# Performance work log

Measured on AMD Instinct MI355X. Metric: run time of the kernel, lower is better.

The kernel has to match this reference:

```python
import jax, jax.numpy as jnp
import numpy as np

N_SRC0, N_DST0 = 400000, 100000
N_DST1 = 25000


def _graph_conv(x_src, src, dst, n_dst, W, b):
    # DGL GraphConv, norm='both': h_v = d_in(v)^-1/2 * sum_{u->v} d_out(u)^-1/2 * x_u @ W + b
    ones = jnp.ones(src.shape[0], dtype=x_src.dtype)
    out_deg = jax.ops.segment_sum(ones, src, num_segments=x_src.shape[0])
    in_deg = jax.ops.segment_sum(ones, dst, num_segments=n_dst)
    cs = jnp.where(out_deg > 0, out_deg ** -0.5, 0.0).astype(x_src.dtype)
    cd = jnp.where(in_deg > 0, in_deg ** -0.5, 0.0).astype(x_src.dtype)
    msg = (x_src * cs[:, None])[src]                      # [E, d_in] gather
    agg = jax.ops.segment_sum(msg, dst, num_segments=n_dst)  # [n_dst, d_in] scatter-add
    return (agg * cd[:, None]) @ W + b


def setup_inputs() -> dict:
    key = jax.random.key(0)
    ks = jax.random.split(key, 8)
    E0, E1 = 3200000, 800000
    return {
        "x": jax.random.normal(ks[0], (N_SRC0, 128), dtype=jnp.float32),
        "src0": jax.random.randint(ks[1], (E0,), 0, N_SRC0, dtype=jnp.int32),
        "dst0": jax.random.randint(ks[2], (E0,), 0, N_DST0, dtype=jnp.int32),
        "src1": jax.random.randint(ks[3], (E1,), 0, N_DST0, dtype=jnp.int32),
        "dst1": jax.random.randint(ks[4], (E1,), 0, N_DST1, dtype=jnp.int32),
        "W0": jax.random.normal(ks[5], (128, 256), dtype=jnp.float32) * (128 ** -0.5),
        "b0": jnp.zeros((256,), dtype=jnp.float32),
        "W1": jax.random.normal(ks[6], (256, 64), dtype=jnp.float32) * (256 ** -0.5),
        "b1": jnp.zeros((64,), dtype=jnp.float32),
    }


def reference(x, src0, dst0, src1, dst1, W0, b0, W1, b1):
    h = jax.nn.relu(_graph_conv(x, src0, dst0, N_DST0, W0, b0))   # [N_DST0, 256]
    h = jax.nn.relu(_graph_conv(h, src1, dst1, N_DST1, W1, b1))   # [N_DST1, 64]
    return h
```

## Files before the change

### kernel.cpp

```cpp
#include <hip/hip_runtime.h>
#include <hip/hip_bf16.h>
#include <stdint.h>

#define N_SRC0 400000
#define N_DST0 100000
#define N_DST1 25000

#define SH_D0 9
#define NK_D0 196
#define SH_S0 9
#define NK_S0 782
#define SH_D1 8
#define NK_D1 98
#define SH_S1 9
#define NK_S1 196
#define NB0 1024
#define NB1 256

#define BH_D0 0
#define BH_S0 (NK_D0 * NB0)
#define BH_D1 (BH_S0 + NK_S0 * NB0)
#define BH_S1 (BH_D1 + NK_D1 * NB1)
#define BH_TOT (BH_S1 + NK_S1 * NB1)

typedef __attribute__((ext_vector_type(8))) short short8;
typedef __attribute__((ext_vector_type(4))) float f32x4;

__device__ __forceinline__ unsigned short f2bf(float f) {
    __hip_bfloat16 h = __float2bfloat16(f);
    union { __hip_bfloat16 h; unsigned short u; } c;
    c.h = h;
    return c.u;
}
__device__ __forceinline__ float bfu_lo(uint32_t u) { return __uint_as_float(u << 16); }
__device__ __forceinline__ float bfu_hi(uint32_t u) { return __uint_as_float(u & 0xffff0000u); }
__device__ __forceinline__ uint32_t packbf2(float a, float b) {
    return (uint32_t)f2bf(a) | ((uint32_t)f2bf(b) << 16);
}

__global__ __launch_bounds__(256) void part_hist2(
        const int* __restrict__ src, const int* __restrict__ dst, int n,
        int sshift, int snb, int dshift, int dnb, int NB,
        int* __restrict__ bhd, int* __restrict__ bhs) {
    extern __shared__ int h[];
    const int blk = blockIdx.x;
    for (int i = threadIdx.x; i < dnb + snb; i += 256) h[i] = 0;
    __syncthreads();
    const int per = (n + NB - 1) / NB;
    const int b = blk * per;
    const int e = min(b + per, n);
    for (int i = b + threadIdx.x; i < e; i += 256) {
        atomicAdd(&h[dst[i] >> dshift], 1);
        atomicAdd(&h[dnb + (src[i] >> sshift)], 1);
    }
    __syncthreads();
    for (int i = threadIdx.x; i < dnb; i += 256) bhd[(size_t)i * NB + blk] = h[i];
    for (int i = threadIdx.x; i < snb; i += 256) bhs[(size_t)i * NB + blk] = h[dnb + i];
}

#define SCAN_ITEMS 8
#define SCAN_TILE 2048

__global__ __launch_bounds__(256) void scan1_kernel(
        const int* __restrict__ in, int* __restrict__ out,
        int* __restrict__ sums, int n) {
    __shared__ int lds[256];
    const int tid = threadIdx.x;
    const int base = blockIdx.x * SCAN_TILE + tid * SCAN_ITEMS;
    int v[SCAN_ITEMS];
    int run = 0;
    #pragma unroll
    for (int i = 0; i < SCAN_ITEMS; ++i) {
        int t = (base + i < n) ? in[base + i] : 0;
        v[i] = run;
        run += t;
    }
    lds[tid] = run;
    __syncthreads();
    int incl = run;
    for (int off = 1; off < 256; off <<= 1) {
        int u = (tid >= off) ? lds[tid - off] : 0;
        __syncthreads();
        incl += u;
        lds[tid] = incl;
        __syncthreads();
    }
    if (tid == 255) sums[blockIdx.x] = incl;
    int excl = incl - run;
    #pragma unroll
    for (int i = 0; i < SCAN_ITEMS; ++i)
        if (base + i < n) out[base + i] = excl + v[i];
}

__global__ __launch_bounds__(256) void scan2_kernel(int* __restrict__ sums, int nb) {
    __shared__ int lds[256];
    const int tid = threadIdx.x;
    const int base = tid * 4;
    int v[4];
    int run = 0;
    #pragma unroll
    for (int i = 0; i < 4; ++i) {
        int t = (base + i < nb) ? sums[base + i] : 0;
        v[i] = run;
        run += t;
    }
    lds[tid] = run;
    __syncthreads();
    int incl = run;
    for (int off = 1; off < 256; off <<= 1) {
        int u = (tid >= off) ? lds[tid - off] : 0;
        __syncthreads();
        incl += u;
        lds[tid] = incl;
        __syncthreads();
    }
    int excl = incl - run;
    #pragma unroll
    for (int i = 0; i < 4; ++i)
        if (base + i < nb) sums[base + i] = excl + v[i];
}

__global__ void scan3_kernel(int* __restrict__ out, const int* __restrict__ sums, int n) {
    int i = blockIdx.x * blockDim.x + threadIdx.x;
    if (i < n) out[i] += sums[i / SCAN_TILE];
}

__global__ __launch_bounds__(256) void part_scat2(
        const int* __restrict__ src, const int* __restrict__ dst, int n,
        int sshift, int snb, int dshift, int dnb, int NB,
        const int* __restrict__ bhd, const int* __restrict__ bhs,
        uint64_t* __restrict__ stg) {
    extern __shared__ int cur[];
    const int blk = blockIdx.x;
    for (int i = threadIdx.x; i < dnb; i += 256) cur[i] = bhd[(size_t)i * NB + blk];
    for (int i = threadIdx.x; i < snb; i += 256) cur[dnb + i] = bhs[(size_t)i * NB + blk];
    __syncthreads();
    const int per = (n + NB - 1) / NB;
    const int b = blk * per;
    const int e = min(b + per, n);
    for (int i = b + threadIdx.x; i < e; i += 256) {
        int s = src[i], d = dst[i];
        int pd = atomicAdd(&cur[d >> dshift], 1);
        stg[pd] = ((uint64_t)(uint32_t)d << 32) | (uint32_t)s;
        int ps = atomicAdd(&cur[dnb + (s >> sshift)], 1);
        stg[ps] = ((uint64_t)(uint32_t)s << 32);
    }
}

__global__ __launch_bounds__(256) void fine_csr(
        const uint64_t* __restrict__ stg, const int* __restrict__ bhs,
        int NB, int shift, int nbins, int total, int rel,
        int* __restrict__ off, int* __restrict__ esrc) {
    __shared__ int fine[512];
    __shared__ int part[256];
    const int k = blockIdx.x;
    const int fb = 1 << shift;
    const int base = bhs[(size_t)k * NB];
    const int end = (k + 1 < gridDim.x) ? bhs[(size_t)(k + 1) * NB] : total;
    const int gb = k << shift;
    const int t = threadIdx.x;
    for (int i = t; i < fb; i += 256) fine[i] = 0;
    __syncthreads();
    for (int i = base + t; i < end; i += 256)
        atomicAdd(&fine[(int)(stg[i] >> 32) - gb], 1);
    __syncthreads();
    int a0 = (2 * t < fb) ? fine[2 * t] : 0;
    int a1 = (2 * t + 1 < fb) ? fine[2 * t + 1] : 0;
    part[t] = a0 + a1;
    __syncthreads();
    int incl = part[t];
    for (int o = 1; o < 256; o <<= 1) {
        int u = (t >= o) ? part[t - o] : 0;
        __syncthreads();
        incl += u;
        part[t] = incl;
        __syncthreads();
    }
    int excl = incl - (a0 + a1);
    if (2 * t < fb) fine[2 * t] = excl;
    if (2 * t + 1 < fb) fine[2 * t + 1] = excl + a0;
    __syncthreads();
    const int rb = base - rel;
    for (int i = t; i < fb; i += 256) {
        int g = gb + i;
        if (g < nbins) off[g] = rb + fine[i];
    }
    if (k == gridDim.x - 1 && t == 0) off[nbins] = total - rel;
    __syncthreads();
    for (int i = base + t; i < end; i += 256) {
        uint64_t pr = stg[i];
        int d = (int)(pr >> 32);
        int p = atomicAdd(&fine[d - gb], 1);
        esrc[rb + p] = (int)(uint32_t)pr;
    }
}

__global__ __launch_bounds__(256) void fine_hist(
        const uint64_t* __restrict__ stg, const int* __restrict__ bhs,
        int NB, int shift, int nbins, int total, float* __restrict__ cs) {
    __shared__ int fine[512];
    const int k = blockIdx.x;
    const int fb = 1 << shift;
    const int base = bhs[(size_t)k * NB];
    const int end = (k + 1 < gridDim.x) ? bhs[(size_t)(k + 1) * NB] : total;
    const int gb = k << shift;
    for (int i = threadIdx.x; i < fb; i += 256) fine[i] = 0;
    __syncthreads();
    for (int i = base + threadIdx.x; i < end; i += 256)
        atomicAdd(&fine[(int)(stg[i] >> 32) - gb], 1);
    __syncthreads();
    for (int i = threadIdx.x; i < fb; i += 256) {
        int g = gb + i;
        if (g < nbins) {
            int c = fine[i];
            cs[g] = c > 0 ? rsqrtf((float)c) : 0.f;
        }
    }
}

__global__ __launch_bounds__(256) void prescale_kernel(
        const float4* __restrict__ x4, const float* __restrict__ cs,
        uint2* __restrict__ xs) {
    int id = blockIdx.x * 256 + threadIdx.x;
    int row = id >> 5;
    float c = cs[row];
    float4 v = x4[id];
    uint2 o;
    o.x = packbf2(v.x * c, v.y * c);
    o.y = packbf2(v.z * c, v.w * c);
    xs[id] = o;
}

__global__ void packW0_kernel(const float* __restrict__ W, unsigned short* __restrict__ Bp) {
    int id = blockIdx.x * 256 + threadIdx.x;
    int kk = id & 31, n = (id >> 5) & 255, kt = id >> 13;
    Bp[id] = f2bf(W[(kt * 32 + kk) * 256 + n]);
}
__global__ void packW1_kernel(const float* __restrict__ W, unsigned short* __restrict__ Bp) {
    int id = blockIdx.x * 256 + threadIdx.x;
    int kk = id & 31, n = (id >> 5) & 63, kt = id >> 11;
    Bp[id] = f2bf(W[(kt * 32 + kk) * 64 + n]);
}

__global__ __launch_bounds__(256) void agg0_kernel(
        const uint32_t* __restrict__ xs, const int* __restrict__ esrc,
        const int* __restrict__ off, uint32_t* __restrict__ aggb, int nrows) {
    int row = blockIdx.x * 4 + (threadIdx.x >> 6);
    int t = threadIdx.x & 63;
    if (row >= nrows) return;
    int b = off[row], e = off[row + 1];
    float a0 = 0.f, a1 = 0.f;
    int i = b;
    for (; i + 7 < e; i += 8) {
        int s0 = esrc[i],     s1 = esrc[i + 1], s2 = esrc[i + 2], s3 = esrc[i + 3];
        int s4 = esrc[i + 4], s5 = esrc[i + 5], s6 = esrc[i + 6], s7 = esrc[i + 7];
        uint32_t u0 = xs[(size_t)s0 * 64 + t];
        uint32_t u1 = xs[(size_t)s1 * 64 + t];
        uint32_t u2 = xs[(size_t)s2 * 64 + t];
        uint32_t u3 = xs[(size_t)s3 * 64 + t];
        uint32_t u4 = xs[(size_t)s4 * 64 + t];
        uint32_t u5 = xs[(size_t)s5 * 64 + t];
        uint32_t u6 = xs[(size_t)s6 * 64 + t];
        uint32_t u7 = xs[(size_t)s7 * 64 + t];
        a0 += ((bfu_lo(u0) + bfu_lo(u1)) + (bfu_lo(u2) + bfu_lo(u3)))
            + ((bfu_lo(u4) + bfu_lo(u5)) + (bfu_lo(u6) + bfu_lo(u7)));
        a1 += ((bfu_hi(u0) + bfu_hi(u1)) + (bfu_hi(u2) + bfu_hi(u3)))
            + ((bfu_hi(u4) + bfu_hi(u5)) + (bfu_hi(u6) + bfu_hi(u7)));
    }
    for (; i < e; ++i) {
        uint32_t u = xs[(size_t)esrc[i] * 64 + t];
        a0 += bfu_lo(u);
        a1 += bfu_hi(u);
    }
    float cd = (e > b) ? rsqrtf((float)(e - b)) : 0.f;
    aggb[(size_t)row * 64 + t] = packbf2(a0 * cd, a1 * cd);
}

__global__ __launch_bounds__(256) void gemm0_mfma(
        const short* __restrict__ A,
        const short* __restrict__ Bp,
        const float* __restrict__ bias,
        unsigned short* __restrict__ H) {
    const int w = threadIdx.x >> 6;
    const int l = threadIdx.x & 63;
    const int rbase = blockIdx.x * 32;
    const int cbase = w * 64;
    const int lr = l & 15;
    const int lk = (l >> 4) * 8;
    f32x4 acc[2][4] = {};
    #pragma unroll
    for (int kt = 0; kt < 4; ++kt) {
        short8 a[2], b[4];
        #pragma unroll
        for (int rt = 0; rt < 2; ++rt)
            a[rt] = *(const short8*)(A + (size_t)(rbase + rt * 16 + lr) * 128 + kt * 32 + lk);
        #pragma unroll
        for (int ct = 0; ct < 4; ++ct)
            b[ct] = *(const short8*)(Bp + (size_t)(kt * 256 + cbase + ct * 16 + lr) * 32 + lk);
        #pragma unroll
        for (int rt = 0; rt < 2; ++rt)
            #pragma unroll
            for (int ct = 0; ct < 4; ++ct)
                acc[rt][ct] = __builtin_amdgcn_mfma_f32_16x16x32_bf16(a[rt], b[ct], acc[rt][ct], 0, 0, 0);
    }
    const int orow0 = (l >> 4) * 4;
    #pragma unroll
    for (int rt = 0; rt < 2; ++rt) {
        #pragma unroll
        for (int ct = 0; ct < 4; ++ct) {
            int col = cbase + ct * 16 + lr;
            float bv = bias[col];
            #pragma unroll
            for (int j = 0; j < 4; ++j) {
                int row = rbase + rt * 16 + orow0 + j;
                float v = fmaxf(acc[rt][ct][j] + bv, 0.f);
                H[(size_t)row * 256 + col] = f2bf(v);
            }
        }
    }
}

__global__ __launch_bounds__(256) void gemmt_mfma(
        const short* __restrict__ A,
        const short* __restrict__ Bp,
        const float* __restrict__ cs1,
        unsigned short* __restrict__ Y,
        int M) {
    const int w = threadIdx.x >> 6;
    const int l = threadIdx.x & 63;
    const int rbase = blockIdx.x * 128 + w * 32;
    const int lr = l & 15;
    const int lk = (l >> 4) * 8;
    f32x4 acc[2][4] = {};
    #pragma unroll
    for (int kt = 0; kt < 8; ++kt) {
        short8 a[2], b[4];
        #pragma unroll
        for (int rt = 0; rt < 2; ++rt)
            a[rt] = *(const short8*)(A + (size_t)(rbase + rt * 16 + lr) * 256 + kt * 32 + lk);
        #pragma unroll
        for (int ct = 0; ct < 4; ++ct)
            b[ct] = *(const short8*)(Bp + (size_t)(kt * 64 + ct * 16 + lr) * 32 + lk);
        #pragma unroll
        for (int rt = 0; rt < 2; ++rt)
            #pragma unroll
            for (int ct = 0; ct < 4; ++ct)
                acc[rt][ct] = __builtin_amdgcn_mfma_f32_16x16x32_bf16(a[rt], b[ct], acc[rt][ct], 0, 0, 0);
    }
    const int orow0 = (l >> 4) * 4;
    #pragma unroll
    for (int rt = 0; rt < 2; ++rt) {
        #pragma unroll
        for (int j = 0; j < 4; ++j) {
            int row = rbase + rt * 16 + orow0 + j;
            if (row < M) {
                float c = cs1[row];
                #pragma unroll
                for (int ct = 0; ct < 4; ++ct) {
                    int col = ct * 16 + lr;
                    Y[(size_t)row * 64 + col] = f2bf(acc[rt][ct][j] * c);
                }
            }
        }
    }
}

__global__ __launch_bounds__(256) void agg1_kernel(
        const uint32_t* __restrict__ y, const int* __restrict__ esrc,
        const int* __restrict__ off, const float* __restrict__ bias,
        float* __restrict__ out, int nrows) {
    int row = blockIdx.x * 8 + (threadIdx.x >> 5);
    int t = threadIdx.x & 31;
    if (row >= nrows) return;
    int b = off[row], e = off[row + 1];
    float a0 = 0.f, a1 = 0.f;
    int i = b;
    for (; i + 3 < e; i += 4) {
        int s0 = esrc[i], s1 = esrc[i + 1], s2 = esrc[i + 2], s3 = esrc[i + 3];
        uint32_t u0 = y[(size_t)s0 * 32 + t];
        uint32_t u1 = y[(size_t)s1 * 32 + t];
        uint32_t u2 = y[(size_t)s2 * 32 + t];
        uint32_t u3 = y[(size_t)s3 * 32 + t];
        a0 += (bfu_lo(u0) + bfu_lo(u1)) + (bfu_lo(u2) + bfu_lo(u3));
        a1 += (bfu_hi(u0) + bfu_hi(u1)) + (bfu_hi(u2) + bfu_hi(u3));
    }
    for (; i < e; ++i) {
        uint32_t u = y[(size_t)esrc[i] * 32 + t];
        a0 += bfu_lo(u);
        a1 += bfu_hi(u);
    }
    float cd = (e > b) ? rsqrtf((float)(e - b)) : 0.f;
    float2 o;
    o.x = fmaxf(a0 * cd + bias[t * 2], 0.f);
    o.y = fmaxf(a1 * cd + bias[t * 2 + 1], 0.f);
    *(float2*)(out + (size_t)row * 64 + t * 2) = o;
}

extern "C" void kernel_launch(void* const* d_in, const int* in_sizes, int n_in,
                              void* d_out, int out_size, void* d_ws, size_t ws_size,
                              hipStream_t stream) {
    const float* x    = (const float*)d_in[0];
    const int*   src0 = (const int*)d_in[1];
    const int*   dst0 = (const int*)d_in[2];
    const int*   src1 = (const int*)d_in[3];
    const int*   dst1 = (const int*)d_in[4];
    const float* W0   = (const float*)d_in[5];
    const float* b0   = (const float*)d_in[6];
    const float* W1   = (const float*)d_in[7];
    const float* b1   = (const float*)d_in[8];
    float* out = (float*)d_out;

    const int E0 = in_sizes[1];
    const int E1 = in_sizes[3];
    const int M_PAD = 100096;

    const int T_D0 = E0;
    const int T_S0 = 2 * E0;
    const int T_D1 = 2 * E0 + E1;
    const int T_S1 = 2 * E0 + 2 * E1;

    char* p = (char*)d_ws;
    auto alloc = [&](size_t bytes) {
        char* r = p;
        p += (bytes + 511) & ~(size_t)511;
        return r;
    };
    int*   bh    = (int*)alloc((size_t)BH_TOT * 4);
    int*   sums  = (int*)alloc(1024 * 4);
    int*   off0  = (int*)alloc((size_t)(N_DST0 + 1) * 4);
    int*   off1  = (int*)alloc((size_t)(N_DST1 + 1) * 4);
    float* cs0   = (float*)alloc((size_t)N_SRC0 * 4);
    float* cs1   = (float*)alloc((size_t)N_DST0 * 4);
    int*   esrc0 = (int*)alloc((size_t)E0 * 4);
    int*   esrc1 = (int*)alloc((size_t)E1 * 4);
    unsigned short* W0p = (unsigned short*)alloc((size_t)32768 * 2);
    unsigned short* W1p = (unsigned short*)alloc((size_t)16384 * 2);
    size_t bigA = (size_t)N_SRC0 * 128 * 2;
    size_t bigB = (size_t)N_DST0 * 128 * 2;
    size_t bigStg = (size_t)T_S1 * 8;
    size_t bigSz = bigA + bigB;
    if (bigStg > bigSz) bigSz = bigStg;
    char* big = alloc(bigSz);

    uint64_t* stg = (uint64_t*)big;
    uint32_t* xs   = (uint32_t*)big;
    unsigned short* h0b = (unsigned short*)big;
    uint32_t* aggb = (uint32_t*)(big + bigA);
    unsigned short* y1b = (unsigned short*)(big + bigA);

    int* bh_d0 = bh + BH_D0;
    int* bh_s0 = bh + BH_S0;
    int* bh_d1 = bh + BH_D1;
    int* bh_s1 = bh + BH_S1;

    part_hist2<<<NB0, 256, (NK_D0 + NK_S0) * 4, stream>>>(
        src0, dst0, E0, SH_S0, NK_S0, SH_D0, NK_D0, NB0, bh_d0, bh_s0);
    part_hist2<<<NB1, 256, (NK_D1 + NK_S1) * 4, stream>>>(
        src1, dst1, E1, SH_S1, NK_S1, SH_D1, NK_D1, NB1, bh_d1, bh_s1);

    const int nsb = (BH_TOT + SCAN_TILE - 1) / SCAN_TILE;
    scan1_kernel<<<nsb, 256, 0, stream>>>(bh, bh, sums, BH_TOT);
    scan2_kernel<<<1, 256, 0, stream>>>(sums, nsb);
    scan3_kernel<<<(BH_TOT + 255) / 256, 256, 0, stream>>>(bh, sums, BH_TOT);

    part_scat2<<<NB0, 256, (NK_D0 + NK_S0) * 4, stream>>>(
        src0, dst0, E0, SH_S0, NK_S0, SH_D0, NK_D0, NB0, bh_d0, bh_s0, stg);
    part_scat2<<<NB1, 256, (NK_D1 + NK_S1) * 4, stream>>>(
        src1, dst1, E1, SH_S1, NK_S1, SH_D1, NK_D1, NB1, bh_d1, bh_s1, stg);

    fine_csr<<<NK_D0, 256, 0, stream>>>(stg, bh_d0, NB0, SH_D0, N_DST0, T_D0, 0, off0, esrc0);
    fine_hist<<<NK_S0, 256, 0, stream>>>(stg, bh_s0, NB0, SH_S0, N_SRC0, T_S0, cs0);
    fine_csr<<<NK_D1, 256, 0, stream>>>(stg, bh_d1, NB1, SH_D1, N_DST1, T_D1, 2 * E0, off1, esrc1);
    fine_hist<<<NK_S1, 256, 0, stream>>>(stg, bh_s1, NB1, SH_S1, N_DST0, T_S1, cs1);

    packW0_kernel<<<128, 256, 0, stream>>>(W0, W0p);
    packW1_kernel<<<64, 256, 0, stream>>>(W1, W1p);

    prescale_kernel<<<N_SRC0 * 32 / 256, 256, 0, stream>>>((const float4*)x, cs0, (uint2*)xs);

    agg0_kernel<<<N_DST0 / 4, 256, 0, stream>>>(xs, esrc0, off0, aggb, N_DST0);
    gemm0_mfma<<<N_DST0 / 32, 256, 0, stream>>>((const short*)aggb, (const short*)W0p, b0, h0b);

    gemmt_mfma<<<M_PAD / 128, 256, 0, stream>>>((const short*)h0b, (const short*)W1p, cs1, y1b, N_DST0);
    agg1_kernel<<<N_DST1 / 8, 256, 0, stream>>>((const uint32_t*)y1b, esrc1, off1, b1, out, N_DST1);
}
```

Baseline: 467.7 us.

## Fuse preprocessing kernels, shrink staging to 32-bit, use fp16 packed aggregation

```diff
diff --git a/kernel.cpp b/kernel.cpp
--- a/kernel.cpp
+++ b/kernel.cpp
@@ -1,5 +1,6 @@
 #include <hip/hip_runtime.h>
 #include <hip/hip_bf16.h>
+#include <hip/hip_fp16.h>
 #include <stdint.h>
 
 #define N_SRC0 400000
@@ -32,18 +33,17 @@
     c.h = h;
     return c.u;
 }
-__device__ __forceinline__ float bfu_lo(uint32_t u) { return __uint_as_float(u << 16); }
-__device__ __forceinline__ float bfu_hi(uint32_t u) { return __uint_as_float(u & 0xffff0000u); }
 __device__ __forceinline__ uint32_t packbf2(float a, float b) {
     return (uint32_t)f2bf(a) | ((uint32_t)f2bf(b) << 16);
 }
-
-__global__ __launch_bounds__(256) void part_hist2(
+__device__ __forceinline__ __half2 u2h2(uint32_t u) {
+    return __builtin_bit_cast(__half2, u);
+}
+
+__device__ __forceinline__ void hist_body(
         const int* __restrict__ src, const int* __restrict__ dst, int n,
-        int sshift, int snb, int dshift, int dnb, int NB,
-        int* __restrict__ bhd, int* __restrict__ bhs) {
-    extern __shared__ int h[];
-    const int blk = blockIdx.x;
+        int sshift, int snb, int dshift, int dnb, int NB, int blk,
+        int* __restrict__ bhd, int* __restrict__ bhs, int* h) {
     for (int i = threadIdx.x; i < dnb + snb; i += 256) h[i] = 0;
     __syncthreads();
     const int per = (n + NB - 1) / NB;
@@ -56,6 +56,19 @@
     __syncthreads();
     for (int i = threadIdx.x; i < dnb; i += 256) bhd[(size_t)i * NB + blk] = h[i];
     for (int i = threadIdx.x; i < snb; i += 256) bhs[(size_t)i * NB + blk] = h[dnb + i];
+}
+
+__global__ __launch_bounds__(256) void hist_fused(
+        const int* __restrict__ src0, const int* __restrict__ dst0, int E0,
+        const int* __restrict__ src1, const int* __restrict__ dst1, int E1,
+        int* __restrict__ bh) {
+    extern __shared__ int h[];
+    if (blockIdx.x < NB0)
+        hist_body(src0, dst0, E0, SH_S0, NK_S0, SH_D0, NK_D0, NB0, blockIdx.x,
+                  bh + BH_D0, bh + BH_S0, h);
+    else
+        hist_body(src1, dst1, E1, SH_S1, NK_S1, SH_D1, NK_D1, NB1, blockIdx.x - NB0,
+                  bh + BH_D1, bh + BH_S1, h);
 }
 
 #define SCAN_ITEMS 8
@@ -125,44 +138,54 @@
     if (i < n) out[i] += sums[i / SCAN_TILE];
 }
 
-__global__ __launch_bounds__(256) void part_scat2(
+__device__ __forceinline__ void scat_body(
         const int* __restrict__ src, const int* __restrict__ dst, int n,
-        int sshift, int snb, int dshift, int dnb, int NB,
+        int sshift, int snb, int dshift, int dnb, int NB, int blk, int ksh,
         const int* __restrict__ bhd, const int* __restrict__ bhs,
-        uint64_t* __restrict__ stg) {
-    extern __shared__ int cur[];
-    const int blk = blockIdx.x;
+        uint32_t* __restrict__ stg, int* cur) {
     for (int i = threadIdx.x; i < dnb; i += 256) cur[i] = bhd[(size_t)i * NB + blk];
     for (int i = threadIdx.x; i < snb; i += 256) cur[dnb + i] = bhs[(size_t)i * NB + blk];
     __syncthreads();
     const int per = (n + NB - 1) / NB;
     const int b = blk * per;
     const int e = min(b + per, n);
+    const int dmask = (1 << dshift) - 1;
     for (int i = b + threadIdx.x; i < e; i += 256) {
         int s = src[i], d = dst[i];
         int pd = atomicAdd(&cur[d >> dshift], 1);
-        stg[pd] = ((uint64_t)(uint32_t)d << 32) | (uint32_t)s;
+        stg[pd] = ((uint32_t)(d & dmask) << ksh) | (uint32_t)s;
         int ps = atomicAdd(&cur[dnb + (s >> sshift)], 1);
-        stg[ps] = ((uint64_t)(uint32_t)s << 32);
-    }
-}
-
-__global__ __launch_bounds__(256) void fine_csr(
-        const uint64_t* __restrict__ stg, const int* __restrict__ bhs,
-        int NB, int shift, int nbins, int total, int rel,
-        int* __restrict__ off, int* __restrict__ esrc) {
-    __shared__ int fine[512];
-    __shared__ int part[256];
-    const int k = blockIdx.x;
+        stg[ps] = (uint32_t)s;
+    }
+}
+
+__global__ __launch_bounds__(256) void scat_fused(
+        const int* __restrict__ src0, const int* __restrict__ dst0, int E0,
+        const int* __restrict__ src1, const int* __restrict__ dst1, int E1,
+        const int* __restrict__ bh, uint32_t* __restrict__ stg) {
+    extern __shared__ int cur[];
+    if (blockIdx.x < NB0)
+        scat_body(src0, dst0, E0, SH_S0, NK_S0, SH_D0, NK_D0, NB0, blockIdx.x, 19,
+                  bh + BH_D0, bh + BH_S0, stg, cur);
+    else
+        scat_body(src1, dst1, E1, SH_S1, NK_S1, SH_D1, NK_D1, NB1, blockIdx.x - NB0, 17,
+                  bh + BH_D1, bh + BH_S1, stg, cur);
+}
+
+__device__ __forceinline__ void fine_csr_body(
+        const uint32_t* __restrict__ stg, const int* __restrict__ bht,
+        int NB, int shift, int ksh, int nbins, int total, int rel, int nbkt, int k,
+        int* __restrict__ off, int* __restrict__ esrc, int* fine, int* part) {
     const int fb = 1 << shift;
-    const int base = bhs[(size_t)k * NB];
-    const int end = (k + 1 < gridDim.x) ? bhs[(size_t)(k + 1) * NB] : total;
+    const int base = bht[(size_t)k * NB];
+    const int end = (k + 1 < nbkt) ? bht[(size_t)(k + 1) * NB] : total;
     const int gb = k << shift;
     const int t = threadIdx.x;
+    const uint32_t mask = (1u << ksh) - 1;
     for (int i = t; i < fb; i += 256) fine[i] = 0;
     __syncthreads();
     for (int i = base + t; i < end; i += 256)
-        atomicAdd(&fine[(int)(stg[i] >> 32) - gb], 1);
+        atomicAdd(&fine[stg[i] >> ksh], 1);
     __syncthreads();
     int a0 = (2 * t < fb) ? fine[2 * t] : 0;
     int a1 = (2 * t + 1 < fb) ? fine[2 * t + 1] : 0;
@@ -185,95 +208,145 @@
         int g = gb + i;
         if (g < nbins) off[g] = rb + fine[i];
     }
-    if (k == gridDim.x - 1 && t == 0) off[nbins] = total - rel;
+    if (k == nbkt - 1 && t == 0) off[nbins] = total - rel;
     __syncthreads();
     for (int i = base + t; i < end; i += 256) {
-        uint64_t pr = stg[i];
-        int d = (int)(pr >> 32);
-        int p = atomicAdd(&fine[d - gb], 1);
-        esrc[rb + p] = (int)(uint32_t)pr;
-    }
-}
-
-__global__ __launch_bounds__(256) void fine_hist(
-        const uint64_t* __restrict__ stg, const int* __restrict__ bhs,
-        int NB, int shift, int nbins, int total, float* __restrict__ cs) {
-    __shared__ int fine[512];
-    const int k = blockIdx.x;
+        uint32_t v = stg[i];
+        int p = atomicAdd(&fine[v >> ksh], 1);
+        esrc[rb + p] = (int)(v & mask);
+    }
+}
+
+__device__ __forceinline__ void fine_deg_body(
+        const uint32_t* __restrict__ stg, const int* __restrict__ bht,
+        int NB, int shift, int nbins, int total, int nbkt, int k,
+        uint32_t* __restrict__ csp, float* __restrict__ csf, int* fine) {
     const int fb = 1 << shift;
-    const int base = bhs[(size_t)k * NB];
-    const int end = (k + 1 < gridDim.x) ? bhs[(size_t)(k + 1) * NB] : total;
+    const int base = bht[(size_t)k * NB];
+    const int end = (k + 1 < nbkt) ? bht[(size_t)(k + 1) * NB] : total;
     const int gb = k << shift;
     for (int i = threadIdx.x; i < fb; i += 256) fine[i] = 0;
     __syncthreads();
     for (int i = base + threadIdx.x; i < end; i += 256)
-        atomicAdd(&fine[(int)(stg[i] >> 32) - gb], 1);
+        atomicAdd(&fine[(int)stg[i] - gb], 1);
     __syncthreads();
     for (int i = threadIdx.x; i < fb; i += 256) {
         int g = gb + i;
         if (g < nbins) {
             int c = fine[i];
-            cs[g] = c > 0 ? rsqrtf((float)c) : 0.f;
+            float r = c > 0 ? rsqrtf((float)c) : 0.f;
+            if (csp) {
+                __half2 h = __floats2half2_rn(r, r);
+                csp[g] = __builtin_bit_cast(uint32_t, h);
+            } else {
+                csf[g] = r;
+            }
         }
     }
 }
 
-__global__ __launch_bounds__(256) void prescale_kernel(
-        const float4* __restrict__ x4, const float* __restrict__ cs,
-        uint2* __restrict__ xs) {
+__global__ __launch_bounds__(256) void fine_fused(
+        const uint32_t* __restrict__ stg, const int* __restrict__ bh,
+        int E0, int E1,
+        int* __restrict__ off0, int* __restrict__ esrc0,
+        int* __restrict__ off1, int* __restrict__ esrc1,
+        uint32_t* __restrict__ cs0p, float* __restrict__ cs1) {
+    __shared__ int fine[512];
+    __shared__ int part[256];
+    int kb = blockIdx.x;
+    if (kb < NK_D0) {
+        fine_csr_body(stg, bh + BH_D0, NB0, SH_D0, 19, N_DST0, E0, 0, NK_D0, kb,
+                      off0, esrc0, fine, part);
+        return;
+    }
+    kb -= NK_D0;
+    if (kb < NK_S0) {
+        fine_deg_body(stg, bh + BH_S0, NB0, SH_S0, N_SRC0, 2 * E0, NK_S0, kb,
+                      cs0p, nullptr, fine);
+        return;
+    }
+    kb -= NK_S0;
+    if (kb < NK_D1) {
+        fine_csr_body(stg, bh + BH_D1, NB1, SH_D1, 17, N_DST1, 2 * E0 + E1, 2 * E0, NK_D1, kb,
+                      off1, esrc1, fine, part);
+        return;
+    }
+    kb -= NK_D1;
+    fine_deg_body(stg, bh + BH_S1, NB1, SH_S1, N_DST0, 2 * E0 + 2 * E1, NK_S1, kb,
+                  nullptr, cs1, fine);
+}
+
+__global__ __launch_bounds__(256) void xconv_kernel(
+        const float4* __restrict__ x4, uint2* __restrict__ xs) {
     int id = blockIdx.x * 256 + threadIdx.x;
-    int row = id >> 5;
-    float c = cs[row];
     float4 v = x4[id];
     uint2 o;
-    o.x = packbf2(v.x * c, v.y * c);
-    o.y = packbf2(v.z * c, v.w * c);
+    o.x = __builtin_bit_cast(uint32_t, __floats2half2_rn(v.x, v.y));
+    o.y = __builtin_bit_cast(uint32_t, __floats2half2_rn(v.z, v.w));
     xs[id] = o;
 }
 
-__global__ void packW0_kernel(const float* __restrict__ W, unsigned short* __restrict__ Bp) {
-    int id = blockIdx.x * 256 + threadIdx.x;
-    int kk = id & 31, n = (id >> 5) & 255, kt = id >> 13;
-    Bp[id] = f2bf(W[(kt * 32 + kk) * 256 + n]);
-}
-__global__ void packW1_kernel(const float* __restrict__ W, unsigned short* __restrict__ Bp) {
-    int id = blockIdx.x * 256 + threadIdx.x;
-    int kk = id & 31, n = (id >> 5) & 63, kt = id >> 11;
-    Bp[id] = f2bf(W[(kt * 32 + kk) * 64 + n]);
+__global__ __launch_bounds__(256) void packw_fused(
+        const float* __restrict__ W0, const float* __restrict__ W1,
+        unsigned short* __restrict__ W0p, unsigned short* __restrict__ W1p) {
+    int blk = blockIdx.x;
+    if (blk < 128) {
+        int id = blk * 256 + threadIdx.x;
+        int kk = id & 31, n2 = (id >> 5) & 255, kt = id >> 13;
+        W0p[id] = f2bf(W0[(kt * 32 + kk) * 256 + n2]);
+    } else {
+        int id = (blk - 128) * 256 + threadIdx.x;
+        int kk = id & 31, n2 = (id >> 5) & 63, kt = id >> 11;
+        W1p[id] = f2bf(W1[(kt * 32 + kk) * 64 + n2]);
+    }
 }
 
 __global__ __launch_bounds__(256) void agg0_kernel(
-        const uint32_t* __restrict__ xs, const int* __restrict__ esrc,
-        const int* __restrict__ off, uint32_t* __restrict__ aggb, int nrows) {
-    int row = blockIdx.x * 4 + (threadIdx.x >> 6);
-    int t = threadIdx.x & 63;
-    if (row >= nrows) return;
-    int b = off[row], e = off[row + 1];
-    float a0 = 0.f, a1 = 0.f;
+        const uint4* __restrict__ xs4, const int* __restrict__ esrc,
+        const int* __restrict__ off, const uint32_t* __restrict__ cs0p,
+        uint4* __restrict__ aggb4) {
+    const int row = blockIdx.x * 16 + (threadIdx.x >> 4);
+    const int t = threadIdx.x & 15;
+    const int b = off[row], e = off[row + 1];
+    const __half2 z = __builtin_bit_cast(__half2, 0u);
+    __half2 aA0 = z, aA1 = z, aA2 = z, aA3 = z;
+    __half2 aB0 = z, aB1 = z, aB2 = z, aB3 = z;
     int i = b;
-    for (; i + 7 < e; i += 8) {
-        int s0 = esrc[i],     s1 = esrc[i + 1], s2 = esrc[i + 2], s3 = esrc[i + 3];
-        int s4 = esrc[i + 4], s5 = esrc[i + 5], s6 = esrc[i + 6], s7 = esrc[i + 7];
-        uint32_t u0 = xs[(size_t)s0 * 64 + t];
-        uint32_t u1 = xs[(size_t)s1 * 64 + t];
-        uint32_t u2 = xs[(size_t)s2 * 64 + t];
-        uint32_t u3 = xs[(size_t)s3 * 64 + t];
-        uint32_t u4 = xs[(size_t)s4 * 64 + t];
-        uint32_t u5 = xs[(size_t)s5 * 64 + t];
-        uint32_t u6 = xs[(size_t)s6 * 64 + t];
-        uint32_t u7 = xs[(size_t)s7 * 64 + t];
-        a0 += ((bfu_lo(u0) + bfu_lo(u1)) + (bfu_lo(u2) + bfu_lo(u3)))
-            + ((bfu_lo(u4) + bfu_lo(u5)) + (bfu_lo(u6) + bfu_lo(u7)));
-        a1 += ((bfu_hi(u0) + bfu_hi(u1)) + (bfu_hi(u2) + bfu_hi(u3)))
-            + ((bfu_hi(u4) + bfu_hi(u5)) + (bfu_hi(u6) + bfu_hi(u7)));
+    for (; i + 8 <= e; i += 8) {
+        #pragma unroll
+        for (int k = 0; k < 8; k += 2) {
+            int s0 = esrc[i + k], s1 = esrc[i + k + 1];
+            __half2 c0 = u2h2(cs0p[s0]), c1 = u2h2(cs0p[s1]);
+            uint4 v0 = xs4[(size_t)s0 * 16 + t];
+            uint4 v1 = xs4[(size_t)s1 * 16 + t];
+            aA0 = __hfma2(u2h2(v0.x), c0, aA0);
+            aA1 = __hfma2(u2h2(v0.y), c0, aA1);
+            aA2 = __hfma2(u2h2(v0.z), c0, aA2);
+            aA3 = __hfma2(u2h2(v0.w), c0, aA3);
+            aB0 = __hfma2(u2h2(v1.x), c1, aB0);
+            aB1 = __hfma2(u2h2(v1.y), c1, aB1);
+            aB2 = __hfma2(u2h2(v1.z), c1, aB2);
+            aB3 = __hfma2(u2h2(v1.w), c1, aB3);
+        }
     }
     for (; i < e; ++i) {
-        uint32_t u = xs[(size_t)esrc[i] * 64 + t];
-        a0 += bfu_lo(u);
-        a1 += bfu_hi(u);
+        int s = esrc[i];
+        __half2 c = u2h2(cs0p[s]);
+        uint4 v = xs4[(size_t)s * 16 + t];
+        aA0 = __hfma2(u2h2(v.x), c, aA0);
+        aA1 = __hfma2(u2h2(v.y), c, aA1);
+        aA2 = __hfma2(u2h2(v.z), c, aA2);
+        aA3 = __hfma2(u2h2(v.w), c, aA3);
     }
     float cd = (e > b) ? rsqrtf((float)(e - b)) : 0.f;
-    aggb[(size_t)row * 64 + t] = packbf2(a0 * cd, a1 * cd);
+    __half2 s0 = __hadd2(aA0, aB0), s1 = __hadd2(aA1, aB1);
+    __half2 s2 = __hadd2(aA2, aB2), s3 = __hadd2(aA3, aB3);
+    uint4 o;
+    o.x = packbf2(__low2float(s0) * cd, __high2float(s0) * cd);
+    o.y = packbf2(__low2float(s1) * cd, __high2float(s1) * cd);
+    o.z = packbf2(__low2float(s2) * cd, __high2float(s2) * cd);
+    o.w = packbf2(__low2float(s3) * cd, __high2float(s3) * cd);
+    aggb4[(size_t)row * 16 + t] = o;
 }
 
 __global__ __launch_bounds__(256) void gemm0_mfma(
@@ -324,7 +397,7 @@
         const short* __restrict__ A,
         const short* __restrict__ Bp,
         const float* __restrict__ cs1,
-        unsigned short* __restrict__ Y,
+        __half* __restrict__ Y,
         int M) {
     const int w = threadIdx.x >> 6;
     const int l = threadIdx.x & 63;
@@ -358,7 +431,7 @@
                 #pragma unroll
                 for (int ct = 0; ct < 4; ++ct) {
                     int col = ct * 16 + lr;
-                    Y[(size_t)row * 64 + col] = f2bf(acc[rt][ct][j] * c);
+                    Y[(size_t)row * 64 + col] = __float2half(acc[rt][ct][j] * c);
                 }
             }
         }
@@ -366,34 +439,42 @@
 }
 
 __global__ __launch_bounds__(256) void agg1_kernel(
-        const uint32_t* __restrict__ y, const int* __restrict__ esrc,
+        const uint2* __restrict__ y2, const int* __restrict__ esrc,
         const int* __restrict__ off, const float* __restrict__ bias,
         float* __restrict__ out, int nrows) {
-    int row = blockIdx.x * 8 + (threadIdx.x >> 5);
-    int t = threadIdx.x & 31;
+    int row = blockIdx.x * 16 + (threadIdx.x >> 4);
+    int t = threadIdx.x & 15;
     if (row >= nrows) return;
     int b = off[row], e = off[row + 1];
-    float a0 = 0.f, a1 = 0.f;
+    const __half2 z = __builtin_bit_cast(__half2, 0u);
+    __half2 aA0 = z, aA1 = z, aB0 = z, aB1 = z;
     int i = b;
-    for (; i + 3 < e; i += 4) {
-        int s0 = esrc[i], s1 = esrc[i + 1], s2 = esrc[i + 2], s3 = esrc[i + 3];
-        uint32_t u0 = y[(size_t)s0 * 32 + t];
-        uint32_t u1 = y[(size_t)s1 * 32 + t];
-        uint32_t u2 = y[(size_t)s2 * 32 + t];
-        uint32_t u3 = y[(size_t)s3 * 32 + t];
-        a0 += (bfu_lo(u0) + bfu_lo(u1)) + (bfu_lo(u2) + bfu_lo(u3));
-        a1 += (bfu_hi(u0) + bfu_hi(u1)) + (bfu_hi(u2) + bfu_hi(u3));
+    for (; i + 8 <= e; i += 8) {
+        #pragma unroll
+        for (int k = 0; k < 8; k += 2) {
+            int s0 = esrc[i + k], s1 = esrc[i + k + 1];
+            uint2 v0 = y2[(size_t)s0 * 16 + t];
+            uint2 v1 = y2[(size_t)s1 * 16 + t];
+            aA0 = __hadd2(aA0, u2h2(v0.x));
+            aA1 = __hadd2(aA1, u2h2(v0.y));
+            aB0 = __hadd2(aB0, u2h2(v1.x));
+            aB1 = __hadd2(aB1, u2h2(v1.y));
+        }
     }
     for (; i < e; ++i) {
-        uint32_t u = y[(size_t)esrc[i] * 32 + t];
-        a0 += bfu_lo(u);
-        a1 += bfu_hi(u);
+        uint2 v = y2[(size_t)esrc[i] * 16 + t];
+        aA0 = __hadd2(aA0, u2h2(v.x));
+        aA1 = __hadd2(aA1, u2h2(v.y));
     }
     float cd = (e > b) ? rsqrtf((float)(e - b)) : 0.f;
-    float2 o;
-    o.x = fmaxf(a0 * cd + bias[t * 2], 0.f);
-    o.y = fmaxf(a1 * cd + bias[t * 2 + 1], 0.f);
-    *(float2*)(out + (size_t)row * 64 + t * 2) = o;
+    __half2 s0 = __hadd2(aA0, aB0), s1 = __hadd2(aA1, aB1);
+    float4 bv = *(const float4*)(bias + t * 4);
+    float4 o;
+    o.x = fmaxf(__low2float(s0) * cd + bv.x, 0.f);
+    o.y = fmaxf(__high2float(s0) * cd + bv.y, 0.f);
+    o.z = fmaxf(__low2float(s1) * cd + bv.z, 0.f);
+    o.w = fmaxf(__high2float(s1) * cd + bv.w, 0.f);
+    *(float4*)(out + (size_t)row * 64 + t * 4) = o;
 }
 
 extern "C" void kernel_launch(void* const* d_in, const int* in_sizes, int n_in,
@@ -414,73 +495,57 @@
     const int E1 = in_sizes[3];
     const int M_PAD = 100096;
 
-    const int T_D0 = E0;
-    const int T_S0 = 2 * E0;
-    const int T_D1 = 2 * E0 + E1;
-    const int T_S1 = 2 * E0 + 2 * E1;
-
     char* p = (char*)d_ws;
     auto alloc = [&](size_t bytes) {
         char* r = p;
         p += (bytes + 511) & ~(size_t)511;
         return r;
     };
-    int*   bh    = (int*)alloc((size_t)BH_TOT * 4);
-    int*   sums  = (int*)alloc(1024 * 4);
-    int*   off0  = (int*)alloc((size_t)(N_DST0 + 1) * 4);
-    int*   off1  = (int*)alloc((size_t)(N_DST1 + 1) * 4);
-    float* cs0   = (float*)alloc((size_t)N_SRC0 * 4);
-    float* cs1   = (float*)alloc((size_t)N_DST0 * 4);
-    int*   esrc0 = (int*)alloc((size_t)E0 * 4);
-    int*   esrc1 = (int*)alloc((size_t)E1 * 4);
+    int*      bh    = (int*)alloc((size_t)BH_TOT * 4);
+    int*      sums  = (int*)alloc(1024 * 4);
+    int*      off0  = (int*)alloc((size_t)(N_DST0 + 1) * 4);
+    int*      off1  = (int*)alloc((size_t)(N_DST1 + 1) * 4);
+    uint32_t* cs0p  = (uint32_t*)alloc((size_t)N_SRC0 * 4);
+    float*    cs1   = (float*)alloc((size_t)N_DST0 * 4);
+    int*      esrc0 = (int*)alloc((size_t)E0 * 4);
+    int*      esrc1 = (int*)alloc((size_t)E1 * 4);
     unsigned short* W0p = (unsigned short*)alloc((size_t)32768 * 2);
     unsigned short* W1p = (unsigned short*)alloc((size_t)16384 * 2);
     size_t bigA = (size_t)N_SRC0 * 128 * 2;
     size_t bigB = (size_t)N_DST0 * 128 * 2;
-    size_t bigStg = (size_t)T_S1 * 8;
+    size_t bigStg = (size_t)(2 * E0 + 2 * E1) * 4;
     size_t bigSz = bigA + bigB;
     if (bigStg > bigSz) bigSz = bigStg;
     char* big = alloc(bigSz);
 
-    uint64_t* stg = (uint64_t*)big;
-    uint32_t* xs   = (uint32_t*)big;
+    uint32_t* stg = (uint32_t*)big;
+    uint2*    xs  = (uint2*)big;
     unsigned short* h0b = (unsigned short*)big;
-    uint32_t* aggb = (uint32_t*)(big + bigA);
-    unsigned short* y1b = (unsigned short*)(big + bigA);
-
-    int* bh_d0 = bh + BH_D0;
-    int* bh_s0 = bh + BH_S0;
-    int* bh_d1 = bh + BH_D1;
-    int* bh_s1 = bh + BH_S1;
-
-    part_hist2<<<NB0, 256, (NK_D0 + NK_S0) * 4, stream>>>(
-        src0, dst0, E0, SH_S0, NK_S0, SH_D0, NK_D0, NB0, bh_d0, bh_s0);
-    part_hist2<<<NB1, 256, (NK_D1 + NK_S1) * 4, stream>>>(
-        src1, dst1, E1, SH_S1, NK_S1, SH_D1, NK_D1, NB1, bh_d1, bh_s1);
-
+    char* regB = big + bigA;
+    uint4* aggb4 = (uint4*)regB;
+    __half* y1b  = (__half*)regB;
+
+    hist_fused<<<NB0 + NB1, 256, (NK_D0 + NK_S0) * 4, stream>>>(
+        src0, dst0, E0, src1, dst1, E1, bh);
     const int nsb = (BH_TOT + SCAN_TILE - 1) / SCAN_TILE;
     scan1_kernel<<<nsb, 256, 0, stream>>>(bh, bh, sums, BH_TOT);
     scan2_kernel<<<1, 256, 0, stream>>>(sums, nsb);
     scan3_kernel<<<(BH_TOT + 255) / 256, 256, 0, stream>>>(bh, sums, BH_TOT);
-
-    part_scat2<<<NB0, 256, (NK_D0 + NK_S0) * 4, stream>>>(
-        src0, dst0, E0, SH_S0, NK_S0, SH_D0, NK_D0, NB0, bh_d0, bh_s0, stg);
-    part_scat2<<<NB1, 256, (NK_D1 + NK_S1) * 4, stream>>>(
-        src1, dst1, E1, SH_S1, NK_S1, SH_D1, NK_D1, NB1, bh_d1, bh_s1, stg);
-
-    fine_csr<<<NK_D0, 256, 0, stream>>>(stg, bh_d0, NB0, SH_D0, N_DST0, T_D0, 0, off0, esrc0);
-    fine_hist<<<NK_S0, 256, 0, stream>>>(stg, bh_s0, NB0, SH_S0, N_SRC0, T_S0, cs0);
-    fine_csr<<<NK_D1, 256, 0, stream>>>(stg, bh_d1, NB1, SH_D1, N_DST1, T_D1, 2 * E0, off1, esrc1);
-    fine_hist<<<NK_S1, 256, 0, stream>>>(stg, bh_s1, NB1, SH_S1, N_DST0, T_S1, cs1);
-
-    packW0_kernel<<<128, 256, 0, stream>>>(W0, W0p);
-    packW1_kernel<<<64, 256, 0, stream>>>(W1, W1p);
-
-    prescale_kernel<<<N_SRC0 * 32 / 256, 256, 0, stream>>>((const float4*)x, cs0, (uint2*)xs);
-
-    agg0_kernel<<<N_DST0 / 4, 256, 0, stream>>>(xs, esrc0, off0, aggb, N_DST0);
-    gemm0_mfma<<<N_DST0 / 32, 256, 0, stream>>>((const short*)aggb, (const short*)W0p, b0, h0b);
-
-    gemmt_mfma<<<M_PAD / 128, 256, 0, stream>>>((const short*)h0b, (const short*)W1p, cs1, y1b, N_DST0);
-    agg1_kernel<<<N_DST1 / 8, 256, 0, stream>>>((const uint32_t*)y1b, esrc1, off1, b1, out, N_DST1);
-}
+    scat_fused<<<NB0 + NB1, 256, (NK_D0 + NK_S0) * 4, stream>>>(
+        src0, dst0, E0, src1, dst1, E1, bh, stg);
+    fine_fused<<<NK_D0 + NK_S0 + NK_D1 + NK_S1, 256, 0, stream>>>(
+        stg, bh, E0, E1, off0, esrc0, off1, esrc1, cs0p, cs1);
+
+    packw_fused<<<192, 256, 0, stream>>>(W0, W1, W0p, W1p);
+    xconv_kernel<<<N_SRC0 * 32 / 256, 256, 0, stream>>>((const float4*)x, xs);
+
+    agg0_kernel<<<N_DST0 / 16, 256, 0, stream>>>(
+        (const uint4*)xs, esrc0, off0, cs0p, aggb4);
+    gemm0_mfma<<<N_DST0 / 32, 256, 0, stream>>>(
+        (const short*)aggb4, (const short*)W0p, b0, h0b);
+
+    gemmt_mfma<<<M_PAD / 128, 256, 0, stream>>>(
+        (const short*)h0b, (const short*)W1p, cs1, y1b, N_DST0);
+    agg1_kernel<<<(N_DST1 + 15) / 16, 256, 0, stream>>>(
+        (const uint2*)y1b, esrc1, off1, b1, out, N_DST1);
+}
```

After: 436.6 us. 1.07x faster.
